# Kernel optimization log

Measured on AMD Instinct MI355X. Metric: run time of the kernel, lower is better.

Reference implementation:

```python
import jax, jax.numpy as jnp
import numpy as np

EPS_S = 1e-06
EPS_SUM = 1e-08
EPS_LOG = 1e-08


def gram_eigh_svd(h_flat):
    """h_flat: (B, N, k) float32 -> (S: (B,k) desc, Vh: (B,k,k)).
    SVD of h_flat via eigendecomposition of the k x k gram matrix."""
    G = jnp.einsum('bnk,bnm->bkm', h_flat, h_flat)  # (B, k, k)
    evals, evecs = jnp.linalg.eigh(G)               # ascending eigenvalues
    S = jnp.sqrt(jnp.clip(evals, 0.0, None))[:, ::-1]          # descending
    Vh = jnp.swapaxes(evecs[:, :, ::-1], -2, -1)                # rows = right singular vectors
    return S, Vh


def extract_features(S, Vh):
    """(B,k), (B,k,k) -> (B, 2k+2)."""
    S_safe = jnp.clip(S, EPS_S, None)
    s_norm = S_safe / (jnp.sum(S_safe, axis=-1, keepdims=True) + EPS_SUM)
    vh_diag = jnp.diagonal(Vh, axis1=-2, axis2=-1)                       # (B, k)
    vh_offdiag = jnp.clip(
        jnp.sum(Vh * Vh, axis=(-2, -1)) - jnp.sum(vh_diag * vh_diag, axis=-1),
        0.0, None)[:, None]                                              # (B, 1)
    s_ent = -jnp.sum(s_norm * jnp.log(jnp.clip(s_norm, EPS_LOG, None)),
                     axis=-1, keepdims=True)                             # (B, 1)
    out = jnp.concatenate([s_norm, vh_diag, vh_offdiag, s_ent], axis=-1)
    return jnp.where(jnp.isfinite(out), out, jnp.zeros_like(out))


def setup_inputs() -> dict:
    key = jax.random.key(0)
    k1, k2 = jax.random.split(key)
    B, C, H, W = 64, 512, 64, 64
    k = 24
    x = jax.random.normal(k1, (B, C, H, W), dtype=jnp.float32)
    w_proj = jax.random.normal(k2, (k, C), dtype=jnp.float32) * (1.0 / np.sqrt(C))
    ema_s = jnp.ones((k,), dtype=jnp.float32)
    return {"x": x, "w_proj": w_proj, "ema_s": ema_s}


def reference(x, w_proj, ema_s):
    B, C, H, W = x.shape
    k = w_proj.shape[0]
    # 1x1 conv == per-pixel matmul; go straight to (B, H*W, k)
    h_flat = jnp.einsum('bchw,kc->bhwk', x, w_proj).reshape(B, H * W, k)
    # torch path runs eigh under no_grad / fp32
    S, Vh = gram_eigh_svd(jax.lax.stop_gradient(h_flat.astype(jnp.float32)))
    S = jnp.clip(S, EPS_S, None)
    S = jnp.where(jnp.isfinite(S), S, jnp.ones_like(S))
    Vh = jnp.where(jnp.isfinite(Vh), Vh, jnp.zeros_like(Vh))
    features = extract_features(S, Vh)
    novelty = S - ema_s[None, :]
    return (S, Vh, features, novelty)
```

## Files before the change

### kernel.cpp

```cpp
#include <hip/hip_runtime.h>
#include <math.h>


#define N24 24
#define ZS 25
#define HS 25

__global__ __launch_bounds__(256) void proj_gram_kernel(
    const float* __restrict__ x, const float* __restrict__ w,
    double* __restrict__ partial)
{
    const int b    = blockIdx.x >> 2;
    const int q    = blockIdx.x & 3;
    const int tid  = threadIdx.x;
    const int wv   = tid >> 6;
    const int lane = tid & 63;
    const int n0   = (q << 10) | (tid << 2);
    __shared__ __align__(16) float wl[24 * 512];
    __shared__ float hl[4][256 * HS];
    for (int i2 = tid; i2 < 24 * 512; i2 += 256) wl[i2] = w[i2];
    __syncthreads();

    const float* xb = x + ((size_t)b << 21) + n0;
    float h[4][24];
#pragma unroll
    for (int j = 0; j < 4; ++j)
#pragma unroll
        for (int k = 0; k < 24; ++k) h[j][k] = 0.f;

    float4 cA[8];
#pragma unroll
    for (int t = 0; t < 8; ++t)
        cA[t] = *reinterpret_cast<const float4*>(xb + ((size_t)t << 12));

    for (int c = 0; c < 512; c += 8) {
        float4 cB[8];
        if (c + 8 < 512) {
#pragma unroll
            for (int t = 0; t < 8; ++t)
                cB[t] = *reinterpret_cast<const float4*>(xb + ((size_t)(c + 8 + t) << 12));
        }
#pragma unroll
        for (int sub = 0; sub < 2; ++sub) {
            const float4 a0 = cA[sub * 4 + 0];
            const float4 a1 = cA[sub * 4 + 1];
            const float4 a2 = cA[sub * 4 + 2];
            const float4 a3 = cA[sub * 4 + 3];
            const int cc = c + sub * 4;
#pragma unroll
            for (int k = 0; k < 24; ++k) {
                const float4 wv4 = *reinterpret_cast<const float4*>(&wl[k * 512 + cc]);
                h[0][k] += wv4.x * a0.x + wv4.y * a1.x + wv4.z * a2.x + wv4.w * a3.x;
                h[1][k] += wv4.x * a0.y + wv4.y * a1.y + wv4.z * a2.y + wv4.w * a3.y;
                h[2][k] += wv4.x * a0.z + wv4.y * a1.z + wv4.z * a2.z + wv4.w * a3.z;
                h[3][k] += wv4.x * a0.w + wv4.y * a1.w + wv4.z * a2.w + wv4.w * a3.w;
            }
        }
#pragma unroll
        for (int t = 0; t < 8; ++t) cA[t] = cB[t];
    }

    float* hq = hl[wv];
#pragma unroll
    for (int j = 0; j < 4; ++j)
#pragma unroll
        for (int k = 0; k < 24; ++k)
            hq[((lane << 2) + j) * HS + k] = h[j][k];

    for (int p = lane; p < 300; p += 64) {
        int k = 0, pp = p;
        while (pp >= 24 - k) { pp -= 24 - k; ++k; }
        int m = k + pp;
        double acc = 0.0;
        for (int i2 = 0; i2 < 256; ++i2)
            acc += (double)hq[i2 * HS + k] * (double)hq[i2 * HS + m];
        partial[((size_t)(b * 16 + (q << 2) + wv)) * 300 + p] = acc;
    }
}

__global__ __launch_bounds__(320) void gram_reduce_kernel(
    const double* __restrict__ partial, float* __restrict__ G)
{
    const int b = blockIdx.x;
    const int p = threadIdx.x;
    if (p >= 300) return;
    int k = 0, pp = p;
    while (pp >= 24 - k) { pp -= 24 - k; ++k; }
    int m = k + pp;
    double acc = 0.0;
    for (int t = 0; t < 16; ++t)
        acc += partial[((size_t)(b * 16 + t)) * 300 + p];
    float v = (float)acc;
    G[b * 576 + k * 24 + m] = v;
    G[b * 576 + m * 24 + k] = v;
}

__device__ __forceinline__ float rlf(float v, int l) {
    return __int_as_float(__builtin_amdgcn_readlane(__float_as_int(v), l));
}

__device__ __forceinline__ float lapy2f(float xx, float yy) {
#pragma clang fp contract(off)
    float xa = fabsf(xx), ya = fabsf(yy);
    float w = fmaxf(xa, ya), z = fminf(xa, ya);
    float q = z / w;
    float res = w * sqrtf(1.f + q * q);
    return (z == 0.f) ? w : res;
}

__device__ __forceinline__ void slartg_(float f, float g, float& c, float& s, float& r) {
#pragma clang fp contract(off)
    float f1 = fabsf(f), g1 = fabsf(g);
    const float rtmin_ = 0x1p-63f;
    const float rtmax_ = 1.8446743e+19f;
    bool inr = (f1 > rtmin_) && (f1 < rtmax_) && (g1 > rtmin_) && (g1 < rtmax_);
    if (__builtin_expect(!inr && f != 0.f && g != 0.f, 0)) {
        float u = fminf(3.4028235e+38f, fmaxf(0x1p-126f, fmaxf(f1, g1)));
        float fs = f / u, gs = g / u;
        float d = sqrtf(fs * fs + gs * gs);
        float p = 1.f / d;
        c = fabsf(fs) * p;
        s = gs * copysignf(p, f);
        r = copysignf(d, f) * u;
    } else {
        float d = sqrtf(f * f + g * g);
        float p = 1.f / d;
        float cN = f1 * p;
        float sN = g * copysignf(p, f);
        float rN = copysignf(d, f);
        bool gz = (g == 0.f), fz = (f == 0.f);
        c = gz ? 1.f : (fz ? 0.f : cN);
        s = gz ? 0.f : (fz ? copysignf(1.f, g) : sN);
        r = gz ? f   : (fz ? g1 : rN);
    }
}

__device__ __forceinline__ void slaev2_(float a, float b, float cc,
                                        float& rt1, float& rt2, float& cs1, float& sn1) {
#pragma clang fp contract(off)
    float sm = a + cc, df = a - cc, adf = fabsf(df);
    float tb = b + b, ab = fabsf(tb);
    float acmx, acmn;
    if (fabsf(a) > fabsf(cc)) { acmx = a; acmn = cc; } else { acmx = cc; acmn = a; }
    float rt;
    if (adf > ab)      { float q = ab / adf; rt = adf * sqrtf(1.f + q * q); }
    else if (adf < ab) { float q = adf / ab; rt = ab * sqrtf(1.f + q * q); }
    else               rt = ab * sqrtf(2.f);
    int sgn1;
    if (sm < 0.f)      { rt1 = 0.5f * (sm - rt); sgn1 = -1; rt2 = (acmx / rt1) * acmn - (b / rt1) * b; }
    else if (sm > 0.f) { rt1 = 0.5f * (sm + rt); sgn1 =  1; rt2 = (acmx / rt1) * acmn - (b / rt1) * b; }
    else               { rt1 = 0.5f * rt; rt2 = -0.5f * rt; sgn1 = 1; }
    float cs; int sgn2;
    if (df >= 0.f) { cs = df + rt; sgn2 = 1; } else { cs = df - rt; sgn2 = -1; }
    float acs = fabsf(cs);
    if (acs > ab) { float ct = -tb / cs; sn1 = 1.f / sqrtf(1.f + ct * ct); cs1 = ct * sn1; }
    else {
        if (ab == 0.f) { cs1 = 1.f; sn1 = 0.f; }
        else { float tn = -cs / tb; cs1 = 1.f / sqrtf(1.f + tn * tn); sn1 = tn * cs1; }
    }
    if (sgn1 == sgn2) { float tn = cs1; cs1 = -sn1; sn1 = tn; }
}

#define RD(j)   rlf(dr, (j) - 1)
#define RE(j)   rlf(er, (j) - 1)
#define WD(j,v) { float _v = (v); int _j = (j) - 1; dr = (lane == _j) ? _v : dr; }
#define WE(j,v) { float _v = (v); int _j = (j) - 1; er = (lane == _j) ? _v : er; }

__global__ __launch_bounds__(64) void eigh_tridiag_kernel(
    const float* __restrict__ G, float* __restrict__ Aout,
    float* __restrict__ taug, float* __restrict__ deg)
{
#pragma clang fp contract(off)
    const int b = blockIdx.x;
    const int lane = threadIdx.x;
    const int n = N24;

    __shared__ float A[N24 * N24];
    __shared__ float dl[N24 + 1], el[N24 + 1], tau[N24 + 1];
    __shared__ float hv[N24], hw[N24];

    for (int idx = lane; idx < n * n; idx += 64) A[idx] = G[(size_t)b * n * n + idx];
    __syncthreads();

    for (int i = 0; i < n - 1; ++i) {
        const int mlen = n - 1 - i;
        float alpha = A[(i + 1) + N24 * i];
        float ss = 0.f;
        for (int r = i + 2; r < n; ++r) { float t = A[r + N24 * i]; ss += t * t; }
        float xnorm = sqrtf(ss);
        if (xnorm == 0.f) {
            if (lane == 0) { tau[i + 1] = 0.f; el[i + 1] = alpha; dl[i + 1] = A[i + N24 * i]; }
            __syncthreads();
            continue;
        }
        float beta = -copysignf(lapy2f(alpha, xnorm), alpha);
        float taui = (beta - alpha) / beta;
        float scal = 1.f / (alpha - beta);
        if (lane == 0) { tau[i + 1] = taui; el[i + 1] = beta; }
        __syncthreads();
        if (lane >= i + 2 && lane < n) A[lane + N24 * i] *= scal;
        __syncthreads();
        if (lane < mlen) hv[lane] = (lane == 0) ? 1.f : A[(i + 1 + lane) + N24 * i];
        __syncthreads();
        if (lane < mlen) {
            float acc = 0.f;
            int gr = i + 1 + lane;
            for (int c2 = 0; c2 < mlen; ++c2) {
                int gc = i + 1 + c2;
                float av = (gr >= gc) ? A[gr + N24 * gc] : A[gc + N24 * gr];
                acc += av * hv[c2];
            }
            hw[lane] = taui * acc;
        }
        __syncthreads();
        float dot = 0.f;
        for (int r2 = 0; r2 < mlen; ++r2) dot += hw[r2] * hv[r2];
        float alpha2 = -0.5f * taui * dot;
        __syncthreads();
        if (lane < mlen) hw[lane] += alpha2 * hv[lane];
        __syncthreads();
        if (lane < mlen) {
            for (int c2 = 0; c2 <= lane; ++c2)
                A[(i + 1 + lane) + N24 * (i + 1 + c2)] -= hv[lane] * hw[c2] + hw[lane] * hv[c2];
        }
        __syncthreads();
        if (lane == 0) dl[i + 1] = A[i + N24 * i];
        __syncthreads();
    }
    if (lane == 0) dl[n] = A[(n - 1) + N24 * (n - 1)];
    __syncthreads();

    for (int idx = lane; idx < n * n; idx += 64) Aout[b * 576 + idx] = A[idx];
    if (lane < 24) deg[b * 64 + lane] = dl[lane + 1];
    if (lane < 23) deg[b * 64 + 32 + lane] = el[lane + 1];
    if (lane >= 1 && lane < 24) taug[b * 32 + lane] = tau[lane];
}

__global__ __launch_bounds__(64) void eigh_steqr_kernel(
    const float* __restrict__ deg, float* __restrict__ Zout,
    float* __restrict__ dsort)
{
#pragma clang fp contract(off)
    const int b = blockIdx.x;
    const int lane = threadIdx.x;
    const int n = N24;

    __shared__ float Zl[N24 * ZS];

    for (int idx = lane; idx < N24 * ZS; idx += 64) Zl[idx] = 0.f;
    __syncthreads();
    if (lane < n) Zl[lane + ZS * lane] = 1.f;
    __syncthreads();

    float dr = (lane < 24) ? deg[b * 64 + lane] : 0.f;
    float er = (lane < 23) ? deg[b * 64 + 32 + lane] : 0.f;

    {
        const float eps_    = 0x1p-24f;
        const float eps2_   = 0x1p-48f;
        const float safmin_ = 0x1p-126f;
        const float ssfmax_ = 3.0744573e+18f;
        const float ssfmin_ = 0x1p-15f;
        const int nmaxit = n * 30;
        int jtot = 0, l1 = 1;
        int l = 0, lsv = 0, lend = 0, lendsv = 0, mb = 0, iscale = 0;
        float anorm = 0.f, p = 0.f, g = 0.f, r_ = 0.f, c_ = 0.f, s_ = 0.f, f_ = 0.f, b_ = 0.f;
        float rt1 = 0.f, rt2 = 0.f, cc = 0.f, sn = 0.f;
        int m_ = 0, i_ = 0;

L10:
        if (l1 > n) goto L160;
        if (l1 > 1) WE(l1 - 1, 0.f);
        {
            float dnx = __shfl_down(dr, 1, 64);
            float ae = fabsf(er);
            bool inr = (lane >= l1 - 1) && (lane <= n - 2);
            bool t0 = inr && (ae == 0.f);
            bool t1 = inr && (ae <= (sqrtf(fabsf(dr)) * sqrtf(fabsf(dnx))) * eps_);
            unsigned long long msk0 = __ballot(t0);
            unsigned long long mskc = msk0 | __ballot(t1);
            if (mskc) {
                int bit = __builtin_ctzll(mskc);
                m_ = bit + 1;
                bool wasz = (msk0 >> bit) & 1ull;
                if (!wasz) WE(m_, 0.f);
            } else m_ = n;
        }
        l = l1; lsv = l; lend = m_; lendsv = lend; l1 = m_ + 1;
        if (lend == l) goto L10;

        {
            bool ind = (lane >= l - 1) && (lane <= lend - 1);
            bool ine = (lane >= l - 1) && (lane <= lend - 2);
            float v = fmaxf(ind ? fabsf(dr) : 0.f, ine ? fabsf(er) : 0.f);
            for (int off = 32; off; off >>= 1) v = fmaxf(v, __shfl_xor(v, off, 64));
            anorm = v;
        }
        iscale = 0;
        if (anorm == 0.f) goto L10;
        if (anorm > ssfmax_) {
            iscale = 1;
            float mul = ssfmax_ / anorm;
            if (lane + 1 >= l && lane + 1 <= lend) dr *= mul;
            if (lane + 1 >= l && lane + 1 <= lend - 1) er *= mul;
        } else if (anorm < ssfmin_) {
            iscale = 2;
            float mul = ssfmin_ / anorm;
            if (lane + 1 >= l && lane + 1 <= lend) dr *= mul;
            if (lane + 1 >= l && lane + 1 <= lend - 1) er *= mul;
        }
        if (fabsf(RD(lend)) < fabsf(RD(l))) { lend = lsv; l = lendsv; }

        if (lend > l) {
L40:
            if (l != lend) {
                float dnx = __shfl_down(dr, 1, 64);
                bool inr = (lane >= l - 1) && (lane <= lend - 2);
                bool t = inr && (er * er <= (eps2_ * fabsf(dr)) * fabsf(dnx) + safmin_);
                unsigned long long msk = __ballot(t);
                m_ = msk ? (__builtin_ctzll(msk) + 1) : lend;
            } else m_ = lend;
            if (m_ < lend) WE(m_, 0.f);
            mb = m_;
            p = RD(l);
            if (mb == l) goto L80;
            if (mb == l + 1) {
                slaev2_(RD(l), RE(l), RD(l + 1), rt1, rt2, cc, sn);
                if (lane < n) {
                    float z1 = Zl[lane + ZS * l];
                    float z0 = Zl[lane + ZS * (l - 1)];
                    Zl[lane + ZS * l]       = cc * z1 - sn * z0;
                    Zl[lane + ZS * (l - 1)] = sn * z1 + cc * z0;
                }
                WD(l, rt1); WD(l + 1, rt2); WE(l, 0.f);
                l = l + 2;
                if (l <= lend) goto L40;
                goto L140;
            }
            if (jtot == nmaxit) goto L140;
            jtot = jtot + 1;
            {
                float dmb = RD(mb);
                g = (RD(l + 1) - p) / (2.f * RE(l));
                r_ = lapy2f(g, 1.f);
                g = dmb - p + (RE(l) / (g + copysignf(r_, g)));
                s_ = 1.f; c_ = 1.f; p = 0.f;
                float dcar = dmb;
                float carry = (lane < n) ? Zl[lane + ZS * (mb - 1)] : 0.f;
                for (i_ = mb - 1; i_ >= l; --i_) {
                    float ei = RE(i_);
                    float di = RD(i_);
                    f_ = s_ * ei;
                    b_ = c_ * ei;
                    slartg_(g, f_, c_, s_, r_);
                    er = ((i_ != mb - 1) && (lane == i_)) ? r_ : er;
                    g = dcar - p;
                    r_ = (di - g) * s_ + 2.f * c_ * b_;
                    p = s_ * r_;
                    dr = (lane == i_) ? (g + p) : dr;
                    g = c_ * r_ - b_;
                    dcar = di;
                    if (lane < n) {
                        float sj = -s_;
                        float prev = Zl[lane + ZS * (i_ - 1)];
                        Zl[lane + ZS * i_] = c_ * carry - sj * prev;
                        carry = sj * carry + c_ * prev;
                    }
                }
                if (lane < n) Zl[lane + ZS * (l - 1)] = carry;
                WD(l, dcar - p);
                WE(l, g);
            }
            goto L40;
L80:
            WD(l, p);
            l = l + 1;
            if (l <= lend) goto L40;
            goto L140;
        } else {
L90:
            if (l != lend) {
                float epu = __shfl_up(er, 1, 64);
                float dup = __shfl_up(dr, 1, 64);
                bool inr = (lane >= lend) && (lane <= l - 1);
                bool t = inr && (epu * epu <= (eps2_ * fabsf(dr)) * fabsf(dup) + safmin_);
                unsigned long long msk = __ballot(t);
                if (msk) {
                    m_ = 63 - __builtin_clzll(msk) + 1;
                } else m_ = lend;
            } else m_ = lend;
            if (m_ > lend) WE(m_ - 1, 0.f);
            mb = m_;
            p = RD(l);
            if (mb == l) goto L130;
            if (mb == l - 1) {
                slaev2_(RD(l - 1), RE(l - 1), RD(l), rt1, rt2, cc, sn);
                if (lane < n) {
                    float z1 = Zl[lane + ZS * (l - 1)];
                    float z0 = Zl[lane + ZS * (l - 2)];
                    Zl[lane + ZS * (l - 1)] = cc * z1 - sn * z0;
                    Zl[lane + ZS * (l - 2)] = sn * z1 + cc * z0;
                }
                WD(l - 1, rt1); WD(l, rt2); WE(l - 1, 0.f);
                l = l - 2;
                if (l >= lend) goto L90;
                goto L140;
            }
            if (jtot == nmaxit) goto L140;
            jtot = jtot + 1;
            {
                float dmb = RD(mb);
                g = (RD(l - 1) - p) / (2.f * RE(l - 1));
                r_ = lapy2f(g, 1.f);
                g = dmb - p + (RE(l - 1) / (g + copysignf(r_, g)));
                s_ = 1.f; c_ = 1.f; p = 0.f;
                float dcar = dmb;
                float carryPrev = (lane < n) ? Zl[lane + ZS * (mb - 1)] : 0.f;
                for (i_ = mb; i_ <= l - 1; ++i_) {
                    float ei = RE(i_);
                    float dnx = RD(i_ + 1);
                    f_ = s_ * ei;
                    b_ = c_ * ei;
                    slartg_(g, f_, c_, s_, r_);
                    er = ((i_ != mb) && (lane == i_ - 2)) ? r_ : er;
                    g = dcar - p;
                    r_ = (dnx - g) * s_ + 2.f * c_ * b_;
                    p = s_ * r_;
                    dr = (lane == i_ - 1) ? (g + p) : dr;
                    g = c_ * r_ - b_;
                    dcar = dnx;
                    if (lane < n) {
                        float t = Zl[lane + ZS * i_];
                        Zl[lane + ZS * (i_ - 1)] = s_ * t + c_ * carryPrev;
                        carryPrev = c_ * t - s_ * carryPrev;
                    }
                }
                if (lane < n) Zl[lane + ZS * (l - 1)] = carryPrev;
                WD(l, dcar - p);
                WE(l - 1, g);
            }
            goto L90;
L130:
            WD(l, p);
            l = l - 1;
            if (l >= lend) goto L90;
            goto L140;
        }
L140:
        if (iscale == 1) {
            float mul = anorm / ssfmax_;
            if (lane + 1 >= lsv && lane + 1 <= lendsv) dr *= mul;
            if (lane + 1 >= lsv && lane + 1 <= lendsv - 1) er *= mul;
        } else if (iscale == 2) {
            float mul = anorm / ssfmin_;
            if (lane + 1 >= lsv && lane + 1 <= lendsv) dr *= mul;
            if (lane + 1 >= lsv && lane + 1 <= lendsv - 1) er *= mul;
        }
        if (jtot < nmaxit) goto L10;
        goto L160;

L160:
        for (int ii = 2; ii <= n; ++ii) {
            int ia = ii - 1;
            float val = (lane >= ii - 2 && lane <= n - 1) ? dr : __builtin_inff();
            int idx = lane + 1;
            for (int off = 32; off; off >>= 1) {
                float v2 = __shfl_xor(val, off, 64);
                int   i2 = __shfl_xor(idx, off, 64);
                bool take = (v2 < val) || ((v2 == val) && (i2 < idx));
                val = take ? v2 : val;
                idx = take ? i2 : idx;
            }
            int ka = idx;
            float pp = val;
            if (ka != ia) {
                float dia = RD(ia);
                WD(ka, dia);
                WD(ia, pp);
                if (lane < n) {
                    float t = Zl[lane + ZS * (ia - 1)];
                    Zl[lane + ZS * (ia - 1)] = Zl[lane + ZS * (ka - 1)];
                    Zl[lane + ZS * (ka - 1)] = t;
                }
            }
        }
    }
    __syncthreads();

    for (int idx = lane; idx < N24 * ZS; idx += 64) Zout[b * (N24 * ZS) + idx] = Zl[idx];
    if (lane < 24) dsort[b * 32 + lane] = dr;
}

__global__ __launch_bounds__(64) void eigh_back_feat_kernel(
    const float* __restrict__ Ain, const float* __restrict__ taug,
    const float* __restrict__ Zin, const float* __restrict__ dsort,
    const float* __restrict__ ema, float* __restrict__ out)
{
#pragma clang fp contract(off)
    const int b = blockIdx.x;
    const int lane = threadIdx.x;
    const int n = N24;

    __shared__ float A[N24 * N24];
    __shared__ float Zl[N24 * ZS];
    __shared__ float dl[N24 + 1], tau[N24 + 1];
    __shared__ float Sarr[N24], snorm[N24];

    for (int idx = lane; idx < n * n; idx += 64) A[idx] = Ain[b * 576 + idx];
    for (int idx = lane; idx < N24 * ZS; idx += 64) Zl[idx] = Zin[b * (N24 * ZS) + idx];
    if (lane >= 1 && lane < 24) tau[lane] = taug[b * 32 + lane];
    if (lane < 24) dl[lane + 1] = dsort[b * 32 + lane];
    __syncthreads();

    for (int i = n - 2; i >= 0; --i) {
        float taui = tau[i + 1];
        if (taui != 0.f && lane < n) {
            int j = lane;
            float w_ = Zl[(i + 1) + ZS * j];
            for (int r = i + 2; r < n; ++r) w_ += A[r + N24 * i] * Zl[r + ZS * j];
            Zl[(i + 1) + ZS * j] -= taui * w_;
            for (int r = i + 2; r < n; ++r) Zl[r + ZS * j] -= taui * (A[r + N24 * i] * w_);
        }
        __syncthreads();
    }

    const int S_OFF = 0, VH_OFF = 1536, F_OFF = 38400, NOV_OFF = 41600;
    if (lane < n) {
        float ev = dl[n - lane];
        float s0 = sqrtf(fmaxf(ev, 0.f));
        s0 = fmaxf(s0, 1e-6f);
        if (!isfinite(s0)) s0 = 1.f;
        Sarr[lane] = s0;
    }
    __syncthreads();
    if (lane < n) {
        out[S_OFF + b * 24 + lane] = Sarr[lane];
        out[NOV_OFF + b * 24 + lane] = Sarr[lane] - ema[lane];
    }
    for (int idx = lane; idx < 576; idx += 64) {
        int j = idx / 24, i2 = idx % 24;
        float vv = Zl[i2 + ZS * (23 - j)];
        if (!isfinite(vv)) vv = 0.f;
        out[VH_OFF + b * 576 + idx] = vv;
    }
    float sum_ = 0.f;
    for (int j2 = 0; j2 < n; ++j2) sum_ += Sarr[j2];
    float denom = sum_ + 1e-8f;
    if (lane < n) snorm[lane] = Sarr[lane] / denom;
    __syncthreads();
    float ent = 0.f;
    for (int j2 = 0; j2 < n; ++j2) {
        float sn2 = snorm[j2];
        ent -= sn2 * logf(fmaxf(sn2, 1e-8f));
    }
    float sumsq = 0.f, diagsq = 0.f;
    for (int j2 = 0; j2 < n; ++j2)
        for (int i2 = 0; i2 < n; ++i2) { float z = Zl[i2 + ZS * j2]; sumsq += z * z; }
    for (int j2 = 0; j2 < n; ++j2) { float dv = Zl[j2 + ZS * (23 - j2)]; diagsq += dv * dv; }
    float offd = fmaxf(sumsq - diagsq, 0.f);
    if (lane < n) {
        float v0 = snorm[lane]; if (!isfinite(v0)) v0 = 0.f;
        out[F_OFF + b * 50 + lane] = v0;
        float dv = Zl[lane + ZS * (23 - lane)]; if (!isfinite(dv)) dv = 0.f;
        out[F_OFF + b * 50 + 24 + lane] = dv;
    }
    if (lane == 0) {
        if (!isfinite(offd)) offd = 0.f;
        if (!isfinite(ent)) ent = 0.f;
        out[F_OFF + b * 50 + 48] = offd;
        out[F_OFF + b * 50 + 49] = ent;
    }
}

extern "C" void kernel_launch(void* const* d_in, const int* in_sizes, int n_in,
                              void* d_out, int out_size, void* d_ws, size_t ws_size,
                              hipStream_t stream)
{
    const float* x   = (const float*)d_in[0];
    const float* w   = (const float*)d_in[1];
    const float* ema = (const float*)d_in[2];
    float* out = (float*)d_out;

    char* wsb = (char*)d_ws;
    double* partial = (double*)(wsb + 0);
    float*  G       = (float*)(wsb + 2457600);
    float*  Aout    = (float*)(wsb + 2605056);
    float*  taug    = (float*)(wsb + 2752512);
    float*  deg     = (float*)(wsb + 2760704);
    float*  Zout    = (float*)(wsb + 2777088);
    float*  dsort   = (float*)(wsb + 2930688);

    hipLaunchKernelGGL(proj_gram_kernel, dim3(256), dim3(256), 0, stream, x, w, partial);
    hipLaunchKernelGGL(gram_reduce_kernel, dim3(64), dim3(320), 0, stream, partial, G);
    hipLaunchKernelGGL(eigh_tridiag_kernel, dim3(64), dim3(64), 0, stream, G, Aout, taug, deg);
    hipLaunchKernelGGL(eigh_steqr_kernel, dim3(64), dim3(64), 0, stream, deg, Zout, dsort);
    hipLaunchKernelGGL(eigh_back_feat_kernel, dim3(64), dim3(64), 0, stream, Aout, taug, Zout, dsort, ema, out);
}
```

Baseline: 492.6 us.

## Fuse tridiagonalization, QR iteration and back-transform into one eigh kernel; deepen x prefetch

Merges the three per-batch eigensolver kernels into one kernel that keeps A, tau, d/e and Z in shared memory, dropping two launches and the global round trips between them. Z is widened to a 65-column stride so all 64 lanes can update rows without the lane<n guards, and loads in the QR sweep are hoisted ahead of the rotation math. The projection kernel doubles its register prefetch of x to 16 channels per step under launch_bounds(256,1), trading register pressure for more memory-level parallelism.

```diff
diff --git a/kernel.cpp b/kernel.cpp
--- a/kernel.cpp
+++ b/kernel.cpp
@@ -3,10 +3,10 @@
 
 
 #define N24 24
-#define ZS 25
+#define ZST 65
 #define HS 25
 
-__global__ __launch_bounds__(256) void proj_gram_kernel(
+__global__ __launch_bounds__(256, 1) void proj_gram_kernel(
     const float* __restrict__ x, const float* __restrict__ w,
     double* __restrict__ partial)
 {
@@ -28,20 +28,20 @@
 #pragma unroll
         for (int k = 0; k < 24; ++k) h[j][k] = 0.f;
 
-    float4 cA[8];
-#pragma unroll
-    for (int t = 0; t < 8; ++t)
+    float4 cA[16];
+#pragma unroll
+    for (int t = 0; t < 16; ++t)
         cA[t] = *reinterpret_cast<const float4*>(xb + ((size_t)t << 12));
 
-    for (int c = 0; c < 512; c += 8) {
-        float4 cB[8];
-        if (c + 8 < 512) {
-#pragma unroll
-            for (int t = 0; t < 8; ++t)
-                cB[t] = *reinterpret_cast<const float4*>(xb + ((size_t)(c + 8 + t) << 12));
-        }
-#pragma unroll
-        for (int sub = 0; sub < 2; ++sub) {
+    for (int c = 0; c < 512; c += 16) {
+        float4 cB[16];
+        if (c + 16 < 512) {
+#pragma unroll
+            for (int t = 0; t < 16; ++t)
+                cB[t] = *reinterpret_cast<const float4*>(xb + ((size_t)(c + 16 + t) << 12));
+        }
+#pragma unroll
+        for (int sub = 0; sub < 4; ++sub) {
             const float4 a0 = cA[sub * 4 + 0];
             const float4 a1 = cA[sub * 4 + 1];
             const float4 a2 = cA[sub * 4 + 2];
@@ -57,7 +57,7 @@
             }
         }
 #pragma unroll
-        for (int t = 0; t < 8; ++t) cA[t] = cB[t];
+        for (int t = 0; t < 16; ++t) cA[t] = cB[t];
     }
 
     float* hq = hl[wv];
@@ -166,9 +166,9 @@
 #define WD(j,v) { float _v = (v); int _j = (j) - 1; dr = (lane == _j) ? _v : dr; }
 #define WE(j,v) { float _v = (v); int _j = (j) - 1; er = (lane == _j) ? _v : er; }
 
-__global__ __launch_bounds__(64) void eigh_tridiag_kernel(
-    const float* __restrict__ G, float* __restrict__ Aout,
-    float* __restrict__ taug, float* __restrict__ deg)
+__global__ __launch_bounds__(64) void eigh_feat_kernel(
+    const float* __restrict__ G, const float* __restrict__ ema,
+    float* __restrict__ out)
 {
 #pragma clang fp contract(off)
     const int b = blockIdx.x;
@@ -176,8 +176,10 @@
     const int n = N24;
 
     __shared__ float A[N24 * N24];
+    __shared__ float Zl[ZST * N24];
     __shared__ float dl[N24 + 1], el[N24 + 1], tau[N24 + 1];
     __shared__ float hv[N24], hw[N24];
+    __shared__ float Sarr[N24], snorm[N24];
 
     for (int idx = lane; idx < n * n; idx += 64) A[idx] = G[(size_t)b * n * n + idx];
     __syncthreads();
@@ -230,30 +232,11 @@
     if (lane == 0) dl[n] = A[(n - 1) + N24 * (n - 1)];
     __syncthreads();
 
-    for (int idx = lane; idx < n * n; idx += 64) Aout[b * 576 + idx] = A[idx];
-    if (lane < 24) deg[b * 64 + lane] = dl[lane + 1];
-    if (lane < 23) deg[b * 64 + 32 + lane] = el[lane + 1];
-    if (lane >= 1 && lane < 24) taug[b * 32 + lane] = tau[lane];
-}
-
-__global__ __launch_bounds__(64) void eigh_steqr_kernel(
-    const float* __restrict__ deg, float* __restrict__ Zout,
-    float* __restrict__ dsort)
-{
-#pragma clang fp contract(off)
-    const int b = blockIdx.x;
-    const int lane = threadIdx.x;
-    const int n = N24;
-
-    __shared__ float Zl[N24 * ZS];
-
-    for (int idx = lane; idx < N24 * ZS; idx += 64) Zl[idx] = 0.f;
-    __syncthreads();
-    if (lane < n) Zl[lane + ZS * lane] = 1.f;
-    __syncthreads();
-
-    float dr = (lane < 24) ? deg[b * 64 + lane] : 0.f;
-    float er = (lane < 23) ? deg[b * 64 + 32 + lane] : 0.f;
+#pragma unroll
+    for (int j = 0; j < N24; ++j) Zl[lane + ZST * j] = (lane == j) ? 1.f : 0.f;
+
+    float dr = (lane < 24) ? dl[lane + 1] : 0.f;
+    float er = (lane < 23) ? el[lane + 1] : 0.f;
 
     {
         const float eps_    = 0x1p-24f;
@@ -326,11 +309,11 @@
             if (mb == l) goto L80;
             if (mb == l + 1) {
                 slaev2_(RD(l), RE(l), RD(l + 1), rt1, rt2, cc, sn);
-                if (lane < n) {
-                    float z1 = Zl[lane + ZS * l];
-                    float z0 = Zl[lane + ZS * (l - 1)];
-                    Zl[lane + ZS * l]       = cc * z1 - sn * z0;
-                    Zl[lane + ZS * (l - 1)] = sn * z1 + cc * z0;
+                {
+                    float z1 = Zl[lane + ZST * l];
+                    float z0 = Zl[lane + ZST * (l - 1)];
+                    Zl[lane + ZST * l]       = cc * z1 - sn * z0;
+                    Zl[lane + ZST * (l - 1)] = sn * z1 + cc * z0;
                 }
                 WD(l, rt1); WD(l + 1, rt2); WE(l, 0.f);
                 l = l + 2;
@@ -346,8 +329,9 @@
                 g = dmb - p + (RE(l) / (g + copysignf(r_, g)));
                 s_ = 1.f; c_ = 1.f; p = 0.f;
                 float dcar = dmb;
-                float carry = (lane < n) ? Zl[lane + ZS * (mb - 1)] : 0.f;
+                float carry = Zl[lane + ZST * (mb - 1)];
                 for (i_ = mb - 1; i_ >= l; --i_) {
+                    float prev = Zl[lane + ZST * (i_ - 1)];
                     float ei = RE(i_);
                     float di = RD(i_);
                     f_ = s_ * ei;
@@ -360,14 +344,11 @@
                     dr = (lane == i_) ? (g + p) : dr;
                     g = c_ * r_ - b_;
                     dcar = di;
-                    if (lane < n) {
-                        float sj = -s_;
-                        float prev = Zl[lane + ZS * (i_ - 1)];
-                        Zl[lane + ZS * i_] = c_ * carry - sj * prev;
-                        carry = sj * carry + c_ * prev;
-                    }
+                    float sj = -s_;
+                    Zl[lane + ZST * i_] = c_ * carry - sj * prev;
+                    carry = sj * carry + c_ * prev;
                 }
-                if (lane < n) Zl[lane + ZS * (l - 1)] = carry;
+                Zl[lane + ZST * (l - 1)] = carry;
                 WD(l, dcar - p);
                 WE(l, g);
             }
@@ -395,11 +376,11 @@
             if (mb == l) goto L130;
             if (mb == l - 1) {
                 slaev2_(RD(l - 1), RE(l - 1), RD(l), rt1, rt2, cc, sn);
-                if (lane < n) {
-                    float z1 = Zl[lane + ZS * (l - 1)];
-                    float z0 = Zl[lane + ZS * (l - 2)];
-                    Zl[lane + ZS * (l - 1)] = cc * z1 - sn * z0;
-                    Zl[lane + ZS * (l - 2)] = sn * z1 + cc * z0;
+                {
+                    float z1 = Zl[lane + ZST * (l - 1)];
+                    float z0 = Zl[lane + ZST * (l - 2)];
+                    Zl[lane + ZST * (l - 1)] = cc * z1 - sn * z0;
+                    Zl[lane + ZST * (l - 2)] = sn * z1 + cc * z0;
                 }
                 WD(l - 1, rt1); WD(l, rt2); WE(l - 1, 0.f);
                 l = l - 2;
@@ -415,8 +396,9 @@
                 g = dmb - p + (RE(l - 1) / (g + copysignf(r_, g)));
                 s_ = 1.f; c_ = 1.f; p = 0.f;
                 float dcar = dmb;
-                float carryPrev = (lane < n) ? Zl[lane + ZS * (mb - 1)] : 0.f;
+                float carryPrev = Zl[lane + ZST * (mb - 1)];
                 for (i_ = mb; i_ <= l - 1; ++i_) {
+                    float t = Zl[lane + ZST * i_];
                     float ei = RE(i_);
                     float dnx = RD(i_ + 1);
                     f_ = s_ * ei;
@@ -429,13 +411,10 @@
                     dr = (lane == i_ - 1) ? (g + p) : dr;
                     g = c_ * r_ - b_;
                     dcar = dnx;
-                    if (lane < n) {
-                        float t = Zl[lane + ZS * i_];
-                        Zl[lane + ZS * (i_ - 1)] = s_ * t + c_ * carryPrev;
-                        carryPrev = c_ * t - s_ * carryPrev;
-                    }
+                    Zl[lane + ZST * (i_ - 1)] = s_ * t + c_ * carryPrev;
+                    carryPrev = c_ * t - s_ * carryPrev;
                 }
-                if (lane < n) Zl[lane + ZS * (l - 1)] = carryPrev;
+                Zl[lane + ZST * (l - 1)] = carryPrev;
                 WD(l, dcar - p);
                 WE(l - 1, g);
             }
@@ -477,49 +456,26 @@
                 float dia = RD(ia);
                 WD(ka, dia);
                 WD(ia, pp);
-                if (lane < n) {
-                    float t = Zl[lane + ZS * (ia - 1)];
-                    Zl[lane + ZS * (ia - 1)] = Zl[lane + ZS * (ka - 1)];
-                    Zl[lane + ZS * (ka - 1)] = t;
+                {
+                    float t = Zl[lane + ZST * (ia - 1)];
+                    Zl[lane + ZST * (ia - 1)] = Zl[lane + ZST * (ka - 1)];
+                    Zl[lane + ZST * (ka - 1)] = t;
                 }
             }
         }
     }
-    __syncthreads();
-
-    for (int idx = lane; idx < N24 * ZS; idx += 64) Zout[b * (N24 * ZS) + idx] = Zl[idx];
-    if (lane < 24) dsort[b * 32 + lane] = dr;
-}
-
-__global__ __launch_bounds__(64) void eigh_back_feat_kernel(
-    const float* __restrict__ Ain, const float* __restrict__ taug,
-    const float* __restrict__ Zin, const float* __restrict__ dsort,
-    const float* __restrict__ ema, float* __restrict__ out)
-{
-#pragma clang fp contract(off)
-    const int b = blockIdx.x;
-    const int lane = threadIdx.x;
-    const int n = N24;
-
-    __shared__ float A[N24 * N24];
-    __shared__ float Zl[N24 * ZS];
-    __shared__ float dl[N24 + 1], tau[N24 + 1];
-    __shared__ float Sarr[N24], snorm[N24];
-
-    for (int idx = lane; idx < n * n; idx += 64) A[idx] = Ain[b * 576 + idx];
-    for (int idx = lane; idx < N24 * ZS; idx += 64) Zl[idx] = Zin[b * (N24 * ZS) + idx];
-    if (lane >= 1 && lane < 24) tau[lane] = taug[b * 32 + lane];
-    if (lane < 24) dl[lane + 1] = dsort[b * 32 + lane];
+
+    if (lane < 24) dl[lane + 1] = dr;
     __syncthreads();
 
     for (int i = n - 2; i >= 0; --i) {
         float taui = tau[i + 1];
         if (taui != 0.f && lane < n) {
             int j = lane;
-            float w_ = Zl[(i + 1) + ZS * j];
-            for (int r = i + 2; r < n; ++r) w_ += A[r + N24 * i] * Zl[r + ZS * j];
-            Zl[(i + 1) + ZS * j] -= taui * w_;
-            for (int r = i + 2; r < n; ++r) Zl[r + ZS * j] -= taui * (A[r + N24 * i] * w_);
+            float w_ = Zl[(i + 1) + ZST * j];
+            for (int r = i + 2; r < n; ++r) w_ += A[r + N24 * i] * Zl[r + ZST * j];
+            Zl[(i + 1) + ZST * j] -= taui * w_;
+            for (int r = i + 2; r < n; ++r) Zl[r + ZST * j] -= taui * (A[r + N24 * i] * w_);
         }
         __syncthreads();
     }
@@ -539,7 +495,7 @@
     }
     for (int idx = lane; idx < 576; idx += 64) {
         int j = idx / 24, i2 = idx % 24;
-        float vv = Zl[i2 + ZS * (23 - j)];
+        float vv = Zl[i2 + ZST * (23 - j)];
         if (!isfinite(vv)) vv = 0.f;
         out[VH_OFF + b * 576 + idx] = vv;
     }
@@ -555,13 +511,13 @@
     }
     float sumsq = 0.f, diagsq = 0.f;
     for (int j2 = 0; j2 < n; ++j2)
-        for (int i2 = 0; i2 < n; ++i2) { float z = Zl[i2 + ZS * j2]; sumsq += z * z; }
-    for (int j2 = 0; j2 < n; ++j2) { float dv = Zl[j2 + ZS * (23 - j2)]; diagsq += dv * dv; }
+        for (int i2 = 0; i2 < n; ++i2) { float z = Zl[i2 + ZST * j2]; sumsq += z * z; }
+    for (int j2 = 0; j2 < n; ++j2) { float dv = Zl[j2 + ZST * (23 - j2)]; diagsq += dv * dv; }
     float offd = fmaxf(sumsq - diagsq, 0.f);
     if (lane < n) {
         float v0 = snorm[lane]; if (!isfinite(v0)) v0 = 0.f;
         out[F_OFF + b * 50 + lane] = v0;
-        float dv = Zl[lane + ZS * (23 - lane)]; if (!isfinite(dv)) dv = 0.f;
+        float dv = Zl[lane + ZST * (23 - lane)]; if (!isfinite(dv)) dv = 0.f;
         out[F_OFF + b * 50 + 24 + lane] = dv;
     }
     if (lane == 0) {
@@ -584,15 +540,8 @@
     char* wsb = (char*)d_ws;
     double* partial = (double*)(wsb + 0);
     float*  G       = (float*)(wsb + 2457600);
-    float*  Aout    = (float*)(wsb + 2605056);
-    float*  taug    = (float*)(wsb + 2752512);
-    float*  deg     = (float*)(wsb + 2760704);
-    float*  Zout    = (float*)(wsb + 2777088);
-    float*  dsort   = (float*)(wsb + 2930688);
 
     hipLaunchKernelGGL(proj_gram_kernel, dim3(256), dim3(256), 0, stream, x, w, partial);
     hipLaunchKernelGGL(gram_reduce_kernel, dim3(64), dim3(320), 0, stream, partial, G);
-    hipLaunchKernelGGL(eigh_tridiag_kernel, dim3(64), dim3(64), 0, stream, G, Aout, taug, deg);
-    hipLaunchKernelGGL(eigh_steqr_kernel, dim3(64), dim3(64), 0, stream, deg, Zout, dsort);
-    hipLaunchKernelGGL(eigh_back_feat_kernel, dim3(64), dim3(64), 0, stream, Aout, taug, Zout, dsort, ema, out);
-}
+    hipLaunchKernelGGL(eigh_feat_kernel, dim3(64), dim3(64), 0, stream, G, ema, out);
+}
```

Measured after the change: 475.7 us. -3.4%, faster.
